# Kernel optimization log

Measured on AMD Instinct MI355X. Metric: run time of the kernel, lower is better.

Reference implementation:

```python
import jax, jax.numpy as jnp
import numpy as np

B, H, S, D = 2, 8, 2048, 64
WINDOW = 3            # local_attention_window (default in torch forward)
FRAC = 0.3            # percentage_frac hardcoded in create_window_tensor call
MASK_FILL = -1.0e9


def window_kernel(window, frac):
    # create_window_tensor: [ (1-f)^n ... (1-f)^1, 1, (1-f)^1 ... (1-f)^n ]
    n = (window - 1) // 2
    side = np.array([(1.0 - frac) ** i for i in range(n, 0, -1)], dtype=np.float32)
    vals = np.concatenate([side, np.array([1.0], np.float32), side[::-1]])
    return jnp.asarray(vals)


def setup_inputs() -> dict:
    key = jax.random.key(0)
    kq, kk, kv = jax.random.split(key, 3)
    queries = jax.random.normal(kq, (B, H, S, D), jnp.float32)
    keys = jax.random.normal(kk, (B, H, S, D), jnp.float32)
    values = jax.random.normal(kv, (B, H, S, D), jnp.float32)
    # causal mask: True positions are filled with -1e9 (masked_fill semantics)
    mask = jnp.triu(jnp.ones((S, S), dtype=bool), 1)[None, None]  # [1,1,S,S]
    # linear_bias: nn.Parameter(torch.zeros(Sk)) created inside forward
    beta = jnp.zeros((S,), jnp.float32)
    return {"queries": queries, "keys": keys, "values": values,
            "beta": beta, "mask": mask}


def reference(queries, keys, values, beta, mask):
    d = keys.shape[-1]
    # scores = Q K^T / sqrt(d)
    scores = jnp.einsum("bhqd,bhkd->bhqk", queries, keys) / jnp.sqrt(
        jnp.asarray(d, queries.dtype))
    scores = jnp.where(mask, jnp.asarray(MASK_FILL, scores.dtype), scores)
    # include_local_attention=True, local_attention_dim_vertical=False:
    # the torch code transposes, conv2d with a [1,W] kernel along the last
    # axis, transposes back -> 1D cross-correlation along the QUERY axis.
    # Kernel is symmetric so correlation == convolution. Zero padding.
    kern = window_kernel(WINDOW, FRAC)
    p = (WINDOW - 1) // 2
    xp = jnp.pad(scores, ((0, 0), (0, 0), (p, p), (0, 0)))
    Sq = scores.shape[2]
    scores = sum(kern[i] * jax.lax.dynamic_slice_in_dim(xp, i, Sq, axis=2)
                 for i in range(WINDOW))
    # linear_bias=True: add zero-initialized per-key-position bias
    scores = scores + beta  # broadcasts over last dim [Sk]
    weights = jax.nn.softmax(scores, axis=-1)
    return jnp.einsum("bhqk,bhkd->bhqd", weights, values)
```

## Files before the change

kernel.cpp:

```cpp
#include <hip/hip_runtime.h>


typedef short bf16x8 __attribute__((ext_vector_type(8)));
typedef float f32x4  __attribute__((ext_vector_type(4)));

constexpr int S_ = 2048;
constexpr int D_ = 64;
constexpr float LOG2E = 1.44269504088896341f;
constexpr float KSC = 0.125f * LOG2E;

__device__ __forceinline__ unsigned pk2(float lo, float hi) {
    union { float f; unsigned u; } a, b;
    a.f = lo; b.f = hi;
    return __builtin_amdgcn_perm(b.u + 0x8000u, a.u + 0x8000u, 0x07060302u);
}

__global__ __launch_bounds__(256)
void cvt8(const float* __restrict__ K, const float* __restrict__ V,
          unsigned short* __restrict__ F)
{
    __shared__ float T[64][68];

    const int bid = blockIdx.x;
    const int hd = bid & 15, tt = bid >> 4;
    const float* Kt = K + ((size_t)hd * S_ + tt * 64) * D_;
    const float* Vt = V + ((size_t)hd * S_ + tt * 64) * D_;
    unsigned short* Ft = F + (size_t)(hd * 32 + tt) * 8192;

    const int t = threadIdx.x;
    const int key = t >> 2, d0 = (t & 3) << 4;

    {
        const float* vp = Vt + key * D_ + d0;
        #pragma unroll
        for (int i = 0; i < 4; ++i) {
            float4 v4 = *(const float4*)(vp + 4 * i);
            T[d0 + 4 * i + 0][key] = v4.x;
            T[d0 + 4 * i + 1][key] = v4.y;
            T[d0 + 4 * i + 2][key] = v4.z;
            T[d0 + 4 * i + 3][key] = v4.w;
        }
    }

    {
        const float* kp = Kt + key * D_ + d0;
        float4 a = *(const float4*)(kp);
        float4 b = *(const float4*)(kp + 4);
        float4 c = *(const float4*)(kp + 8);
        float4 d = *(const float4*)(kp + 12);
        uint4 w0 = make_uint4(pk2(a.x, a.y), pk2(a.z, a.w), pk2(b.x, b.y), pk2(b.z, b.w));
        uint4 w1 = make_uint4(pk2(c.x, c.y), pk2(c.z, c.w), pk2(d.x, d.y), pk2(d.z, d.w));
        const int r5 = key & 31;
        const int kh = key >> 5, mb = (r5 >> 2) & 1;
        const int n = ((r5 >> 3) << 2) | (r5 & 3);
        const int hh = d0 >> 5, qd0 = (d0 >> 3) & 3;
        const int f0 = (kh << 2) | (mb << 1) | hh;
        *(uint4*)(Ft + f0 * 512 + ((qd0 << 4) | n) * 8)       = w0;
        *(uint4*)(Ft + f0 * 512 + (((qd0 + 1) << 4) | n) * 8) = w1;
    }
    __syncthreads();

    #pragma unroll
    for (int s = 0; s < 2; ++s) {
        const int slot = t + s * 256;
        const int fr = slot >> 6, lane = slot & 63;
        const int kh = fr >> 2, mb = fr & 3, n = lane & 15, qd = lane >> 4;
        const float* row = &T[mb * 16 + n][kh * 32 + qd * 8];
        uint4 w = make_uint4(pk2(row[0], row[1]), pk2(row[2], row[3]),
                             pk2(row[4], row[5]), pk2(row[6], row[7]));
        *(uint4*)(Ft + (8 + fr) * 512 + lane * 8) = w;
    }
}

__global__ __launch_bounds__(512, 2)
void attn9(const float* __restrict__ Q, const float* __restrict__ beta,
           const unsigned short* __restrict__ F, float* __restrict__ out)
{
    __shared__ float slab[2][64][72];

    const int bid = blockIdx.x;
    const int hd = bid & 15;
    const int pr = bid >> 4;

    const float* Qh = Q + (size_t)hd * S_ * D_;
    const unsigned short* Fh = F + (size_t)hd * 32 * 8192;

    const int t = threadIdx.x, lane = t & 63;
    const int wv = t >> 6;
    const int kh = wv & 1, par = (wv >> 1) & 1, qh = wv >> 2;
    const int n_l = lane & 15, qd = lane >> 4;

    const int lo = lane * 8;
    int kfo[2][2], vfo[4];
    #pragma unroll
    for (int mb = 0; mb < 2; ++mb)
        #pragma unroll
        for (int hh = 0; hh < 2; ++hh)
            kfo[mb][hh] = ((kh << 2) | (mb << 1) | hh) * 512 + lo;
    #pragma unroll
    for (int mb = 0; mb < 4; ++mb)
        vfo[mb] = (8 + (kh << 2) + mb) * 512 + lo;

    const int kvo = (kh << 5) + (qd << 3);
    const float* bp = beta + kvo;

    for (int p = 0; p < 2; ++p) {
        const int j = p ? (31 - pr) : pr;
        const int q0 = j << 6;
        const int nt = j + 1;
        const int qbase = q0 + (qh << 5);

        auto ld = [&](int tile, bf16x8 (&ka)[2][2], bf16x8 (&vb)[4], float (&bt)[8]) {
            const unsigned short* fp = Fh + (size_t)tile * 8192;
            ka[0][0] = *(const bf16x8*)(fp + kfo[0][0]);
            ka[0][1] = *(const bf16x8*)(fp + kfo[0][1]);
            ka[1][0] = *(const bf16x8*)(fp + kfo[1][0]);
            ka[1][1] = *(const bf16x8*)(fp + kfo[1][1]);
            #pragma unroll
            for (int mb = 0; mb < 4; ++mb)
                vb[mb] = *(const bf16x8*)(fp + vfo[mb]);
            const float* bq = bp + (tile << 6);
            float4 b0 = *(const float4*)(bq);
            float4 b1 = *(const float4*)(bq + 4);
            bt[0] = b0.x * LOG2E; bt[1] = b0.y * LOG2E;
            bt[2] = b0.z * LOG2E; bt[3] = b0.w * LOG2E;
            bt[4] = b1.x * LOG2E; bt[5] = b1.y * LOG2E;
            bt[6] = b1.z * LOG2E; bt[7] = b1.w * LOG2E;
        };

        bf16x8 qb[2][2];
        #pragma unroll
        for (int ng = 0; ng < 2; ++ng) {
            const int q = qbase + (ng << 4) + n_l;
            const float wp = (q > 0) ? 0.7f : 0.0f;
            const float wn = (q + 1 < S_) ? 0.7f : 0.0f;
            const float* qc = Qh + (size_t)q * D_;
            const float* qpp = qc - ((q > 0) ? D_ : 0);
            const float* qnn = qc + ((q + 1 < S_) ? D_ : 0);
            #pragma unroll
            for (int hh = 0; hh < 2; ++hh) {
                const int d0 = (hh << 5) + (qd << 3);
                float4 c0 = *(const float4*)(qc + d0),  c1 = *(const float4*)(qc + d0 + 4);
                float4 p0 = *(const float4*)(qpp + d0), p1 = *(const float4*)(qpp + d0 + 4);
                float4 n0 = *(const float4*)(qnn + d0), n1 = *(const float4*)(qnn + d0 + 4);
                float e0 = fmaf(wn, n0.x, fmaf(wp, p0.x, c0.x));
                float e1 = fmaf(wn, n0.y, fmaf(wp, p0.y, c0.y));
                float e2 = fmaf(wn, n0.z, fmaf(wp, p0.z, c0.z));
                float e3 = fmaf(wn, n0.w, fmaf(wp, p0.w, c0.w));
                float e4 = fmaf(wn, n1.x, fmaf(wp, p1.x, c1.x));
                float e5 = fmaf(wn, n1.y, fmaf(wp, p1.y, c1.y));
                float e6 = fmaf(wn, n1.z, fmaf(wp, p1.z, c1.z));
                float e7 = fmaf(wn, n1.w, fmaf(wp, p1.w, c1.w));
                union { unsigned u[4]; bf16x8 v; } qu;
                qu.u[0] = pk2(e0, e1); qu.u[1] = pk2(e2, e3);
                qu.u[2] = pk2(e4, e5); qu.u[3] = pk2(e6, e7);
                qb[ng][hh] = qu.v;
            }
        }

        f32x4 o[4][2];
        float l[2] = {0.0f, 0.0f};
        #pragma unroll
        for (int mb = 0; mb < 4; ++mb)
            #pragma unroll
            for (int ng = 0; ng < 2; ++ng) o[mb][ng] = (f32x4){0, 0, 0, 0};

        auto comp = [&](int tile, bf16x8 (&ka)[2][2], bf16x8 (&vb)[4], float (&bt)[8]) {
            const f32x4 zz = {0, 0, 0, 0};
            f32x4 acc[2][2];
            #pragma unroll
            for (int mb = 0; mb < 2; ++mb)
                #pragma unroll
                for (int ng = 0; ng < 2; ++ng) {
                    f32x4 a = __builtin_amdgcn_mfma_f32_16x16x32_bf16(ka[mb][0], qb[ng][0], zz, 0, 0, 0);
                    acc[mb][ng] = __builtin_amdgcn_mfma_f32_16x16x32_bf16(ka[mb][1], qb[ng][1], a, 0, 0, 0);
                }
            const bool dm = (tile == nt - 1);
            const int kk = (tile << 6) + kvo;
            union { unsigned u[4]; bf16x8 v; } pf[2];
            #pragma unroll
            for (int ng = 0; ng < 2; ++ng) {
                const int qr = qbase + (ng << 4) + n_l;
                float pv[8];
                float la = 0.0f;
                #pragma unroll
                for (int jj = 0; jj < 8; ++jj) {
                    const int mb = jj >> 2, r = jj & 3;
                    float sv = fmaf(acc[mb][ng][r], KSC, bt[jj]);
                    if (dm) {
                        const int key = kk + jj;
                        if (!((key < qr) || (qr == 0 && key == 0))) sv = -1.0e30f;
                    }
                    pv[jj] = __builtin_amdgcn_exp2f(sv);
                    la += pv[jj];
                }
                l[ng] += la;
                pf[ng].u[0] = pk2(pv[0], pv[1]);
                pf[ng].u[1] = pk2(pv[2], pv[3]);
                pf[ng].u[2] = pk2(pv[4], pv[5]);
                pf[ng].u[3] = pk2(pv[6], pv[7]);
            }
            #pragma unroll
            for (int mb = 0; mb < 4; ++mb)
                #pragma unroll
                for (int ng = 0; ng < 2; ++ng)
                    o[mb][ng] = __builtin_amdgcn_mfma_f32_16x16x32_bf16(vb[mb], pf[ng].v, o[mb][ng], 0, 0, 0);
        };

        bf16x8 kaA[2][2], vbA[4]; float btA[8];
        bf16x8 kaB[2][2], vbB[4]; float btB[8];
        int it = par;
        if (it < nt) {
            ld(it, kaA, vbA, btA);
            if (it + 2 < nt) ld(it + 2, kaB, vbB, btB);
            while (it + 4 < nt) {
                comp(it, kaA, vbA, btA);
                ld(it + 4, kaA, vbA, btA);
                comp(it + 2, kaB, vbB, btB);
                if (it + 6 < nt) ld(it + 6, kaB, vbB, btB);
                it += 4;
            }
            comp(it, kaA, vbA, btA);
            if (it + 2 < nt) comp(it + 2, kaB, vbB, btB);
        }

        #pragma unroll
        for (int ng = 0; ng < 2; ++ng) {
            l[ng] += __shfl_xor(l[ng], 16);
            l[ng] += __shfl_xor(l[ng], 32);
        }
        __syncthreads();
        if (par == 1) {
            #pragma unroll
            for (int ng = 0; ng < 2; ++ng) {
                const int row = (qh << 5) + (ng << 4) + n_l;
                #pragma unroll
                for (int mb = 0; mb < 4; ++mb)
                    *(float4*)&slab[kh][row][(mb << 4) + (qd << 2)] =
                        make_float4(o[mb][ng][0], o[mb][ng][1], o[mb][ng][2], o[mb][ng][3]);
                if (qd == 0) slab[kh][row][64] = l[ng];
            }
        }
        __syncthreads();
        if (par == 0) {
            #pragma unroll
            for (int ng = 0; ng < 2; ++ng) {
                const int row = (qh << 5) + (ng << 4) + n_l;
                #pragma unroll
                for (int mb = 0; mb < 4; ++mb) {
                    float4 pv4 = *(float4*)&slab[kh][row][(mb << 4) + (qd << 2)];
                    o[mb][ng][0] += pv4.x; o[mb][ng][1] += pv4.y;
                    o[mb][ng][2] += pv4.z; o[mb][ng][3] += pv4.w;
                }
                l[ng] += slab[kh][row][64];
                if (kh == 0) {
                    #pragma unroll
                    for (int mb = 0; mb < 4; ++mb)
                        *(float4*)&slab[0][row][(mb << 4) + (qd << 2)] =
                            make_float4(o[mb][ng][0], o[mb][ng][1], o[mb][ng][2], o[mb][ng][3]);
                    if (qd == 0) slab[0][row][64] = l[ng];
                }
            }
        }
        __syncthreads();
        if (par == 0 && kh == 1) {
            #pragma unroll
            for (int ng = 0; ng < 2; ++ng) {
                const int row = (qh << 5) + (ng << 4) + n_l;
                const float inv = 1.0f / (l[ng] + slab[0][row][64]);
                float* op = out + ((size_t)hd * S_ + q0 + row) * D_ + (qd << 2);
                #pragma unroll
                for (int mb = 0; mb < 4; ++mb) {
                    float4 pv4 = *(float4*)&slab[0][row][(mb << 4) + (qd << 2)];
                    *(float4*)(op + (mb << 4)) =
                        make_float4((o[mb][ng][0] + pv4.x) * inv, (o[mb][ng][1] + pv4.y) * inv,
                                    (o[mb][ng][2] + pv4.z) * inv, (o[mb][ng][3] + pv4.w) * inv);
                }
            }
        }
    }
}

extern "C" void kernel_launch(void* const* d_in, const int* in_sizes, int n_in,
                              void* d_out, int out_size, void* d_ws, size_t ws_size,
                              hipStream_t stream) {
    const float* Q    = (const float*)d_in[0];
    const float* K    = (const float*)d_in[1];
    const float* V    = (const float*)d_in[2];
    const float* beta = (const float*)d_in[3];
    float* out = (float*)d_out;

    unsigned short* F = (unsigned short*)d_ws;

    cvt8<<<dim3(512), 256, 0, stream>>>(K, V, F);
    attn9<<<dim3(256), 512, 0, stream>>>(Q, beta, F, out);
}
```

Before: 116.4 us.

## Split key tiles four ways per wave and stage beta in shared memory

The attention kernel changes how work is split across its 8 waves. Before, waves were divided between two query halves and two key-tile parities. Now every wave covers all 64 queries of the block and the key tiles are split four ways, so each K/V fragment load feeds twice as many MFMAs. The beta bias is pre-scaled once into shared memory rather than loaded from global memory per tile. The causal-mask branch becomes a compile-time template specialisation. The cost is a larger accumulator register footprint, more shared memory (a 3-way partial-sum slab plus the beta array), and a longer reduction across waves at the end.

Result: slower. 148.2 us (+27.3%).

```diff
diff --git a/kernel.cpp b/kernel.cpp
--- a/kernel.cpp
+++ b/kernel.cpp
@@ -8,6 +8,8 @@
 constexpr int D_ = 64;
 constexpr float LOG2E = 1.44269504088896341f;
 constexpr float KSC = 0.125f * LOG2E;
+
+template <bool B> struct BC { static constexpr bool v = B; };
 
 __device__ __forceinline__ unsigned pk2(float lo, float hi) {
     union { float f; unsigned u; } a, b;
@@ -73,10 +75,11 @@
 }
 
 __global__ __launch_bounds__(512, 2)
-void attn9(const float* __restrict__ Q, const float* __restrict__ beta,
-           const unsigned short* __restrict__ F, float* __restrict__ out)
+void attn10(const float* __restrict__ Q, const float* __restrict__ beta,
+            const unsigned short* __restrict__ F, float* __restrict__ out)
 {
-    __shared__ float slab[2][64][72];
+    __shared__ float slab[2][3][64][68];
+    __shared__ float bl[S_];
 
     const int bid = blockIdx.x;
     const int hd = bid & 15;
@@ -87,8 +90,12 @@
 
     const int t = threadIdx.x, lane = t & 63;
     const int wv = t >> 6;
-    const int kh = wv & 1, par = (wv >> 1) & 1, qh = wv >> 2;
+    const int kh = wv & 1, par = wv >> 1;
     const int n_l = lane & 15, qd = lane >> 4;
+
+    #pragma unroll
+    for (int i = 0; i < 4; ++i) bl[t + i * 512] = beta[t + i * 512] * LOG2E;
+    __syncthreads();
 
     const int lo = lane * 8;
     int kfo[2][2], vfo[4];
@@ -102,15 +109,13 @@
         vfo[mb] = (8 + (kh << 2) + mb) * 512 + lo;
 
     const int kvo = (kh << 5) + (qd << 3);
-    const float* bp = beta + kvo;
 
     for (int p = 0; p < 2; ++p) {
         const int j = p ? (31 - pr) : pr;
         const int q0 = j << 6;
         const int nt = j + 1;
-        const int qbase = q0 + (qh << 5);
-
-        auto ld = [&](int tile, bf16x8 (&ka)[2][2], bf16x8 (&vb)[4], float (&bt)[8]) {
+
+        auto ld = [&](int tile, bf16x8 (&ka)[2][2], bf16x8 (&vb)[4]) {
             const unsigned short* fp = Fh + (size_t)tile * 8192;
             ka[0][0] = *(const bf16x8*)(fp + kfo[0][0]);
             ka[0][1] = *(const bf16x8*)(fp + kfo[0][1]);
@@ -119,19 +124,12 @@
             #pragma unroll
             for (int mb = 0; mb < 4; ++mb)
                 vb[mb] = *(const bf16x8*)(fp + vfo[mb]);
-            const float* bq = bp + (tile << 6);
-            float4 b0 = *(const float4*)(bq);
-            float4 b1 = *(const float4*)(bq + 4);
-            bt[0] = b0.x * LOG2E; bt[1] = b0.y * LOG2E;
-            bt[2] = b0.z * LOG2E; bt[3] = b0.w * LOG2E;
-            bt[4] = b1.x * LOG2E; bt[5] = b1.y * LOG2E;
-            bt[6] = b1.z * LOG2E; bt[7] = b1.w * LOG2E;
         };
 
-        bf16x8 qb[2][2];
-        #pragma unroll
-        for (int ng = 0; ng < 2; ++ng) {
-            const int q = qbase + (ng << 4) + n_l;
+        bf16x8 qb[4][2];
+        #pragma unroll
+        for (int ng = 0; ng < 4; ++ng) {
+            const int q = q0 + (ng << 4) + n_l;
             const float wp = (q > 0) ? 0.7f : 0.0f;
             const float wn = (q + 1 < S_) ? 0.7f : 0.0f;
             const float* qc = Qh + (size_t)q * D_;
@@ -158,120 +156,129 @@
             }
         }
 
-        f32x4 o[4][2];
-        float l[2] = {0.0f, 0.0f};
+        f32x4 o[4][4];
+        float l[4] = {0.0f, 0.0f, 0.0f, 0.0f};
         #pragma unroll
         for (int mb = 0; mb < 4; ++mb)
             #pragma unroll
-            for (int ng = 0; ng < 2; ++ng) o[mb][ng] = (f32x4){0, 0, 0, 0};
-
-        auto comp = [&](int tile, bf16x8 (&ka)[2][2], bf16x8 (&vb)[4], float (&bt)[8]) {
+            for (int ng = 0; ng < 4; ++ng) o[mb][ng] = (f32x4){0, 0, 0, 0};
+
+        auto comp = [&](int tile, bf16x8 (&ka)[2][2], bf16x8 (&vb)[4], auto dmc) {
+            constexpr bool DM = decltype(dmc)::v;
+            const int kb = (tile << 6) + kvo;
+            float4 b0 = *(const float4*)&bl[kb];
+            float4 b1 = *(const float4*)&bl[kb + 4];
+            const float bt[8] = {b0.x, b0.y, b0.z, b0.w, b1.x, b1.y, b1.z, b1.w};
             const f32x4 zz = {0, 0, 0, 0};
-            f32x4 acc[2][2];
+            f32x4 acc[2][4];
             #pragma unroll
             for (int mb = 0; mb < 2; ++mb)
                 #pragma unroll
-                for (int ng = 0; ng < 2; ++ng) {
+                for (int ng = 0; ng < 4; ++ng) {
                     f32x4 a = __builtin_amdgcn_mfma_f32_16x16x32_bf16(ka[mb][0], qb[ng][0], zz, 0, 0, 0);
                     acc[mb][ng] = __builtin_amdgcn_mfma_f32_16x16x32_bf16(ka[mb][1], qb[ng][1], a, 0, 0, 0);
                 }
-            const bool dm = (tile == nt - 1);
-            const int kk = (tile << 6) + kvo;
-            union { unsigned u[4]; bf16x8 v; } pf[2];
-            #pragma unroll
-            for (int ng = 0; ng < 2; ++ng) {
-                const int qr = qbase + (ng << 4) + n_l;
+            #pragma unroll
+            for (int ng = 0; ng < 4; ++ng) {
                 float pv[8];
                 float la = 0.0f;
                 #pragma unroll
                 for (int jj = 0; jj < 8; ++jj) {
                     const int mb = jj >> 2, r = jj & 3;
                     float sv = fmaf(acc[mb][ng][r], KSC, bt[jj]);
-                    if (dm) {
-                        const int key = kk + jj;
+                    if constexpr (DM) {
+                        const int qr = q0 + (ng << 4) + n_l;
+                        const int key = kb + jj;
                         if (!((key < qr) || (qr == 0 && key == 0))) sv = -1.0e30f;
                     }
                     pv[jj] = __builtin_amdgcn_exp2f(sv);
                     la += pv[jj];
                 }
                 l[ng] += la;
-                pf[ng].u[0] = pk2(pv[0], pv[1]);
-                pf[ng].u[1] = pk2(pv[2], pv[3]);
-                pf[ng].u[2] = pk2(pv[4], pv[5]);
-                pf[ng].u[3] = pk2(pv[6], pv[7]);
-            }
-            #pragma unroll
-            for (int mb = 0; mb < 4; ++mb)
-                #pragma unroll
-                for (int ng = 0; ng < 2; ++ng)
-                    o[mb][ng] = __builtin_amdgcn_mfma_f32_16x16x32_bf16(vb[mb], pf[ng].v, o[mb][ng], 0, 0, 0);
+                union { unsigned u[4]; bf16x8 v; } pf;
+                pf.u[0] = pk2(pv[0], pv[1]);
+                pf.u[1] = pk2(pv[2], pv[3]);
+                pf.u[2] = pk2(pv[4], pv[5]);
+                pf.u[3] = pk2(pv[6], pv[7]);
+                #pragma unroll
+                for (int mb = 0; mb < 4; ++mb)
+                    o[mb][ng] = __builtin_amdgcn_mfma_f32_16x16x32_bf16(vb[mb], pf.v, o[mb][ng], 0, 0, 0);
+            }
         };
 
-        bf16x8 kaA[2][2], vbA[4]; float btA[8];
-        bf16x8 kaB[2][2], vbB[4]; float btB[8];
+        bf16x8 kaA[2][2], vbA[4];
+        bf16x8 kaB[2][2], vbB[4];
         int it = par;
         if (it < nt) {
-            ld(it, kaA, vbA, btA);
-            if (it + 2 < nt) ld(it + 2, kaB, vbB, btB);
-            while (it + 4 < nt) {
-                comp(it, kaA, vbA, btA);
-                ld(it + 4, kaA, vbA, btA);
-                comp(it + 2, kaB, vbB, btB);
-                if (it + 6 < nt) ld(it + 6, kaB, vbB, btB);
-                it += 4;
-            }
-            comp(it, kaA, vbA, btA);
-            if (it + 2 < nt) comp(it + 2, kaB, vbB, btB);
-        }
-
-        #pragma unroll
-        for (int ng = 0; ng < 2; ++ng) {
+            ld(it, kaA, vbA);
+            if (it + 4 < nt) ld(it + 4, kaB, vbB);
+            while (it + 8 < nt) {
+                comp(it, kaA, vbA, BC<false>{});
+                ld(it + 8, kaA, vbA);
+                comp(it + 4, kaB, vbB, BC<false>{});
+                if (it + 12 < nt) ld(it + 12, kaB, vbB);
+                it += 8;
+            }
+            if (it == nt - 1) comp(it, kaA, vbA, BC<true>{});
+            else              comp(it, kaA, vbA, BC<false>{});
+            if (it + 4 < nt) {
+                if (it + 4 == nt - 1) comp(it + 4, kaB, vbB, BC<true>{});
+                else                  comp(it + 4, kaB, vbB, BC<false>{});
+            }
+        }
+
+        #pragma unroll
+        for (int ng = 0; ng < 4; ++ng) {
             l[ng] += __shfl_xor(l[ng], 16);
             l[ng] += __shfl_xor(l[ng], 32);
         }
         __syncthreads();
-        if (par == 1) {
-            #pragma unroll
-            for (int ng = 0; ng < 2; ++ng) {
-                const int row = (qh << 5) + (ng << 4) + n_l;
+        if (par != 0) {
+            const int si = par - 1;
+            #pragma unroll
+            for (int ng = 0; ng < 4; ++ng) {
+                const int row = (ng << 4) + n_l;
                 #pragma unroll
                 for (int mb = 0; mb < 4; ++mb)
-                    *(float4*)&slab[kh][row][(mb << 4) + (qd << 2)] =
+                    *(float4*)&slab[kh][si][row][(mb << 4) + (qd << 2)] =
                         make_float4(o[mb][ng][0], o[mb][ng][1], o[mb][ng][2], o[mb][ng][3]);
-                if (qd == 0) slab[kh][row][64] = l[ng];
+                if (qd == 0) slab[kh][si][row][64] = l[ng];
             }
         }
         __syncthreads();
         if (par == 0) {
             #pragma unroll
-            for (int ng = 0; ng < 2; ++ng) {
-                const int row = (qh << 5) + (ng << 4) + n_l;
+            for (int ng = 0; ng < 4; ++ng) {
+                const int row = (ng << 4) + n_l;
                 #pragma unroll
                 for (int mb = 0; mb < 4; ++mb) {
-                    float4 pv4 = *(float4*)&slab[kh][row][(mb << 4) + (qd << 2)];
-                    o[mb][ng][0] += pv4.x; o[mb][ng][1] += pv4.y;
-                    o[mb][ng][2] += pv4.z; o[mb][ng][3] += pv4.w;
-                }
-                l[ng] += slab[kh][row][64];
-                if (kh == 0) {
+                    #pragma unroll
+                    for (int si = 0; si < 3; ++si) {
+                        float4 pv4 = *(float4*)&slab[kh][si][row][(mb << 4) + (qd << 2)];
+                        o[mb][ng][0] += pv4.x; o[mb][ng][1] += pv4.y;
+                        o[mb][ng][2] += pv4.z; o[mb][ng][3] += pv4.w;
+                    }
+                }
+                l[ng] += slab[kh][0][row][64] + slab[kh][1][row][64] + slab[kh][2][row][64];
+                if (kh == 1) {
                     #pragma unroll
                     for (int mb = 0; mb < 4; ++mb)
-                        *(float4*)&slab[0][row][(mb << 4) + (qd << 2)] =
+                        *(float4*)&slab[1][0][row][(mb << 4) + (qd << 2)] =
                             make_float4(o[mb][ng][0], o[mb][ng][1], o[mb][ng][2], o[mb][ng][3]);
-                    if (qd == 0) slab[0][row][64] = l[ng];
+                    if (qd == 0) slab[1][0][row][64] = l[ng];
                 }
             }
         }
         __syncthreads();
-        if (par == 0 && kh == 1) {
-            #pragma unroll
-            for (int ng = 0; ng < 2; ++ng) {
-                const int row = (qh << 5) + (ng << 4) + n_l;
-                const float inv = 1.0f / (l[ng] + slab[0][row][64]);
+        if (par == 0 && kh == 0) {
+            #pragma unroll
+            for (int ng = 0; ng < 4; ++ng) {
+                const int row = (ng << 4) + n_l;
+                const float inv = 1.0f / (l[ng] + slab[1][0][row][64]);
                 float* op = out + ((size_t)hd * S_ + q0 + row) * D_ + (qd << 2);
                 #pragma unroll
                 for (int mb = 0; mb < 4; ++mb) {
-                    float4 pv4 = *(float4*)&slab[0][row][(mb << 4) + (qd << 2)];
+                    float4 pv4 = *(float4*)&slab[1][0][row][(mb << 4) + (qd << 2)];
                     *(float4*)(op + (mb << 4)) =
                         make_float4((o[mb][ng][0] + pv4.x) * inv, (o[mb][ng][1] + pv4.y) * inv,
                                     (o[mb][ng][2] + pv4.z) * inv, (o[mb][ng][3] + pv4.w) * inv);
@@ -293,5 +300,5 @@
     unsigned short* F = (unsigned short*)d_ws;
 
     cvt8<<<dim3(512), 256, 0, stream>>>(K, V, F);
-    attn9<<<dim3(256), 512, 0, stream>>>(Q, beta, F, out);
+    attn10<<<dim3(256), 512, 0, stream>>>(Q, beta, F, out);
 }
```

## Split paired query tiles into separate blocks, stage beta in LDS, prefetch only K

Applied to the files above, without the earlier changes.

Each block used to process two query tiles (j and 31-j) back to back. Now every block handles one tile, the grid doubles to 512 blocks, and blocks are ordered so the longest tiles start first. The beta bias is pre-scaled into shared memory once per block. The software pipeline now prefetches only the K fragments for the next tile, while V is loaded inside the compute step. Launch bounds are raised to 4 blocks per CU to increase occupancy, at the cost of register pressure and less latency hiding for the V loads.

Result: slower. 133.1 us (+14.3%).

```diff
diff --git a/kernel.cpp b/kernel.cpp
--- a/kernel.cpp
+++ b/kernel.cpp
@@ -8,6 +8,8 @@
 constexpr int D_ = 64;
 constexpr float LOG2E = 1.44269504088896341f;
 constexpr float KSC = 0.125f * LOG2E;
+
+template <bool B> struct BC { static constexpr bool v = B; };
 
 __device__ __forceinline__ unsigned pk2(float lo, float hi) {
     union { float f; unsigned u; } a, b;
@@ -72,15 +74,20 @@
     }
 }
 
-__global__ __launch_bounds__(512, 2)
-void attn9(const float* __restrict__ Q, const float* __restrict__ beta,
-           const unsigned short* __restrict__ F, float* __restrict__ out)
+__global__ __launch_bounds__(512, 4)
+void attn14(const float* __restrict__ Q, const float* __restrict__ beta,
+            const unsigned short* __restrict__ F, float* __restrict__ out)
 {
     __shared__ float slab[2][64][72];
+    __shared__ float bl[S_];
 
     const int bid = blockIdx.x;
     const int hd = bid & 15;
-    const int pr = bid >> 4;
+    const int rest = bid >> 4;
+    const int j = (rest < 16) ? (31 - 2 * rest) : (2 * (rest - 16));
+
+    const int q0 = j << 6;
+    const int nt = j + 1;
 
     const float* Qh = Q + (size_t)hd * S_ * D_;
     const unsigned short* Fh = F + (size_t)hd * 32 * 8192;
@@ -89,6 +96,11 @@
     const int wv = t >> 6;
     const int kh = wv & 1, par = (wv >> 1) & 1, qh = wv >> 2;
     const int n_l = lane & 15, qd = lane >> 4;
+    const int qbase = q0 + (qh << 5);
+
+    #pragma unroll
+    for (int i = 0; i < 4; ++i) bl[t + i * 512] = beta[t + i * 512] * LOG2E;
+    __syncthreads();
 
     const int lo = lane * 8;
     int kfo[2][2], vfo[4];
@@ -102,180 +114,169 @@
         vfo[mb] = (8 + (kh << 2) + mb) * 512 + lo;
 
     const int kvo = (kh << 5) + (qd << 3);
-    const float* bp = beta + kvo;
-
-    for (int p = 0; p < 2; ++p) {
-        const int j = p ? (31 - pr) : pr;
-        const int q0 = j << 6;
-        const int nt = j + 1;
-        const int qbase = q0 + (qh << 5);
-
-        auto ld = [&](int tile, bf16x8 (&ka)[2][2], bf16x8 (&vb)[4], float (&bt)[8]) {
-            const unsigned short* fp = Fh + (size_t)tile * 8192;
-            ka[0][0] = *(const bf16x8*)(fp + kfo[0][0]);
-            ka[0][1] = *(const bf16x8*)(fp + kfo[0][1]);
-            ka[1][0] = *(const bf16x8*)(fp + kfo[1][0]);
-            ka[1][1] = *(const bf16x8*)(fp + kfo[1][1]);
+
+    auto ld_ka = [&](int tile, bf16x8 (&ka)[2][2]) {
+        const unsigned short* fp = Fh + (size_t)tile * 8192;
+        ka[0][0] = *(const bf16x8*)(fp + kfo[0][0]);
+        ka[0][1] = *(const bf16x8*)(fp + kfo[0][1]);
+        ka[1][0] = *(const bf16x8*)(fp + kfo[1][0]);
+        ka[1][1] = *(const bf16x8*)(fp + kfo[1][1]);
+    };
+
+    bf16x8 qb[2][2];
+    #pragma unroll
+    for (int ng = 0; ng < 2; ++ng) {
+        const int q = qbase + (ng << 4) + n_l;
+        const float wp = (q > 0) ? 0.7f : 0.0f;
+        const float wn = (q + 1 < S_) ? 0.7f : 0.0f;
+        const float* qc = Qh + (size_t)q * D_;
+        const float* qpp = qc - ((q > 0) ? D_ : 0);
+        const float* qnn = qc + ((q + 1 < S_) ? D_ : 0);
+        #pragma unroll
+        for (int hh = 0; hh < 2; ++hh) {
+            const int d0 = (hh << 5) + (qd << 3);
+            float4 c0 = *(const float4*)(qc + d0),  c1 = *(const float4*)(qc + d0 + 4);
+            float4 p0 = *(const float4*)(qpp + d0), p1 = *(const float4*)(qpp + d0 + 4);
+            float4 n0 = *(const float4*)(qnn + d0), n1 = *(const float4*)(qnn + d0 + 4);
+            float e0 = fmaf(wn, n0.x, fmaf(wp, p0.x, c0.x));
+            float e1 = fmaf(wn, n0.y, fmaf(wp, p0.y, c0.y));
+            float e2 = fmaf(wn, n0.z, fmaf(wp, p0.z, c0.z));
+            float e3 = fmaf(wn, n0.w, fmaf(wp, p0.w, c0.w));
+            float e4 = fmaf(wn, n1.x, fmaf(wp, p1.x, c1.x));
+            float e5 = fmaf(wn, n1.y, fmaf(wp, p1.y, c1.y));
+            float e6 = fmaf(wn, n1.z, fmaf(wp, p1.z, c1.z));
+            float e7 = fmaf(wn, n1.w, fmaf(wp, p1.w, c1.w));
+            union { unsigned u[4]; bf16x8 v; } qu;
+            qu.u[0] = pk2(e0, e1); qu.u[1] = pk2(e2, e3);
+            qu.u[2] = pk2(e4, e5); qu.u[3] = pk2(e6, e7);
+            qb[ng][hh] = qu.v;
+        }
+    }
+
+    f32x4 o[4][2];
+    float l[2] = {0.0f, 0.0f};
+    #pragma unroll
+    for (int mb = 0; mb < 4; ++mb)
+        #pragma unroll
+        for (int ng = 0; ng < 2; ++ng) o[mb][ng] = (f32x4){0, 0, 0, 0};
+
+    auto comp = [&](int tile, bf16x8 (&kaC)[2][2], bf16x8 (&kaN)[2][2], auto prc) {
+        constexpr bool PRE = decltype(prc)::v;
+        const int kb = (tile << 6) + kvo;
+        const unsigned short* fp = Fh + (size_t)tile * 8192;
+        bf16x8 vb[4];
+        #pragma unroll
+        for (int mb = 0; mb < 4; ++mb)
+            vb[mb] = *(const bf16x8*)(fp + vfo[mb]);
+        float4 b0 = *(const float4*)&bl[kb];
+        float4 b1 = *(const float4*)&bl[kb + 4];
+        const float bt[8] = {b0.x, b0.y, b0.z, b0.w, b1.x, b1.y, b1.z, b1.w};
+        const f32x4 zz = {0, 0, 0, 0};
+        f32x4 acc[2][2];
+        #pragma unroll
+        for (int mb = 0; mb < 2; ++mb)
+            #pragma unroll
+            for (int ng = 0; ng < 2; ++ng) {
+                f32x4 a = __builtin_amdgcn_mfma_f32_16x16x32_bf16(kaC[mb][0], qb[ng][0], zz, 0, 0, 0);
+                acc[mb][ng] = __builtin_amdgcn_mfma_f32_16x16x32_bf16(kaC[mb][1], qb[ng][1], a, 0, 0, 0);
+            }
+        if constexpr (PRE) ld_ka(tile + 2, kaN);
+        const bool dm = (tile == nt - 1);
+        #pragma unroll
+        for (int ng = 0; ng < 2; ++ng) {
+            const int qr = qbase + (ng << 4) + n_l;
+            float pv[8];
+            float la = 0.0f;
+            #pragma unroll
+            for (int jj = 0; jj < 8; ++jj) {
+                const int mb = jj >> 2, r = jj & 3;
+                float sv = fmaf(acc[mb][ng][r], KSC, bt[jj]);
+                if (dm) {
+                    const int key = kb + jj;
+                    if (!((key < qr) || (qr == 0 && key == 0))) sv = -1.0e30f;
+                }
+                pv[jj] = __builtin_amdgcn_exp2f(sv);
+                la += pv[jj];
+            }
+            l[ng] += la;
+            union { unsigned u[4]; bf16x8 v; } pf;
+            pf.u[0] = pk2(pv[0], pv[1]);
+            pf.u[1] = pk2(pv[2], pv[3]);
+            pf.u[2] = pk2(pv[4], pv[5]);
+            pf.u[3] = pk2(pv[6], pv[7]);
             #pragma unroll
             for (int mb = 0; mb < 4; ++mb)
-                vb[mb] = *(const bf16x8*)(fp + vfo[mb]);
-            const float* bq = bp + (tile << 6);
-            float4 b0 = *(const float4*)(bq);
-            float4 b1 = *(const float4*)(bq + 4);
-            bt[0] = b0.x * LOG2E; bt[1] = b0.y * LOG2E;
-            bt[2] = b0.z * LOG2E; bt[3] = b0.w * LOG2E;
-            bt[4] = b1.x * LOG2E; bt[5] = b1.y * LOG2E;
-            bt[6] = b1.z * LOG2E; bt[7] = b1.w * LOG2E;
-        };
-
-        bf16x8 qb[2][2];
-        #pragma unroll
-        for (int ng = 0; ng < 2; ++ng) {
-            const int q = qbase + (ng << 4) + n_l;
-            const float wp = (q > 0) ? 0.7f : 0.0f;
-            const float wn = (q + 1 < S_) ? 0.7f : 0.0f;
-            const float* qc = Qh + (size_t)q * D_;
-            const float* qpp = qc - ((q > 0) ? D_ : 0);
-            const float* qnn = qc + ((q + 1 < S_) ? D_ : 0);
-            #pragma unroll
-            for (int hh = 0; hh < 2; ++hh) {
-                const int d0 = (hh << 5) + (qd << 3);
-                float4 c0 = *(const float4*)(qc + d0),  c1 = *(const float4*)(qc + d0 + 4);
-                float4 p0 = *(const float4*)(qpp + d0), p1 = *(const float4*)(qpp + d0 + 4);
-                float4 n0 = *(const float4*)(qnn + d0), n1 = *(const float4*)(qnn + d0 + 4);
-                float e0 = fmaf(wn, n0.x, fmaf(wp, p0.x, c0.x));
-                float e1 = fmaf(wn, n0.y, fmaf(wp, p0.y, c0.y));
-                float e2 = fmaf(wn, n0.z, fmaf(wp, p0.z, c0.z));
-                float e3 = fmaf(wn, n0.w, fmaf(wp, p0.w, c0.w));
-                float e4 = fmaf(wn, n1.x, fmaf(wp, p1.x, c1.x));
-                float e5 = fmaf(wn, n1.y, fmaf(wp, p1.y, c1.y));
-                float e6 = fmaf(wn, n1.z, fmaf(wp, p1.z, c1.z));
-                float e7 = fmaf(wn, n1.w, fmaf(wp, p1.w, c1.w));
-                union { unsigned u[4]; bf16x8 v; } qu;
-                qu.u[0] = pk2(e0, e1); qu.u[1] = pk2(e2, e3);
-                qu.u[2] = pk2(e4, e5); qu.u[3] = pk2(e6, e7);
-                qb[ng][hh] = qu.v;
-            }
-        }
-
-        f32x4 o[4][2];
-        float l[2] = {0.0f, 0.0f};
-        #pragma unroll
-        for (int mb = 0; mb < 4; ++mb)
-            #pragma unroll
-            for (int ng = 0; ng < 2; ++ng) o[mb][ng] = (f32x4){0, 0, 0, 0};
-
-        auto comp = [&](int tile, bf16x8 (&ka)[2][2], bf16x8 (&vb)[4], float (&bt)[8]) {
-            const f32x4 zz = {0, 0, 0, 0};
-            f32x4 acc[2][2];
-            #pragma unroll
-            for (int mb = 0; mb < 2; ++mb)
-                #pragma unroll
-                for (int ng = 0; ng < 2; ++ng) {
-                    f32x4 a = __builtin_amdgcn_mfma_f32_16x16x32_bf16(ka[mb][0], qb[ng][0], zz, 0, 0, 0);
-                    acc[mb][ng] = __builtin_amdgcn_mfma_f32_16x16x32_bf16(ka[mb][1], qb[ng][1], a, 0, 0, 0);
-                }
-            const bool dm = (tile == nt - 1);
-            const int kk = (tile << 6) + kvo;
-            union { unsigned u[4]; bf16x8 v; } pf[2];
-            #pragma unroll
-            for (int ng = 0; ng < 2; ++ng) {
-                const int qr = qbase + (ng << 4) + n_l;
-                float pv[8];
-                float la = 0.0f;
-                #pragma unroll
-                for (int jj = 0; jj < 8; ++jj) {
-                    const int mb = jj >> 2, r = jj & 3;
-                    float sv = fmaf(acc[mb][ng][r], KSC, bt[jj]);
-                    if (dm) {
-                        const int key = kk + jj;
-                        if (!((key < qr) || (qr == 0 && key == 0))) sv = -1.0e30f;
-                    }
-                    pv[jj] = __builtin_amdgcn_exp2f(sv);
-                    la += pv[jj];
-                }
-                l[ng] += la;
-                pf[ng].u[0] = pk2(pv[0], pv[1]);
-                pf[ng].u[1] = pk2(pv[2], pv[3]);
-                pf[ng].u[2] = pk2(pv[4], pv[5]);
-                pf[ng].u[3] = pk2(pv[6], pv[7]);
-            }
+                o[mb][ng] = __builtin_amdgcn_mfma_f32_16x16x32_bf16(vb[mb], pf.v, o[mb][ng], 0, 0, 0);
+        }
+    };
+
+    bf16x8 kaA[2][2], kaB[2][2];
+    int it = par;
+    if (it < nt) {
+        ld_ka(it, kaA);
+        while (it + 4 < nt) {
+            comp(it,     kaA, kaB, BC<true>{});
+            comp(it + 2, kaB, kaA, BC<true>{});
+            it += 4;
+        }
+        if (it + 2 < nt) {
+            comp(it,     kaA, kaB, BC<true>{});
+            comp(it + 2, kaB, kaA, BC<false>{});
+        } else {
+            comp(it, kaA, kaB, BC<false>{});
+        }
+    }
+
+    #pragma unroll
+    for (int ng = 0; ng < 2; ++ng) {
+        l[ng] += __shfl_xor(l[ng], 16);
+        l[ng] += __shfl_xor(l[ng], 32);
+    }
+    if (par == 1) {
+        #pragma unroll
+        for (int ng = 0; ng < 2; ++ng) {
+            const int row = (qh << 5) + (ng << 4) + n_l;
             #pragma unroll
             for (int mb = 0; mb < 4; ++mb)
-                #pragma unroll
-                for (int ng = 0; ng < 2; ++ng)
-                    o[mb][ng] = __builtin_amdgcn_mfma_f32_16x16x32_bf16(vb[mb], pf[ng].v, o[mb][ng], 0, 0, 0);
-        };
-
-        bf16x8 kaA[2][2], vbA[4]; float btA[8];
-        bf16x8 kaB[2][2], vbB[4]; float btB[8];
-        int it = par;
-        if (it < nt) {
-            ld(it, kaA, vbA, btA);
-            if (it + 2 < nt) ld(it + 2, kaB, vbB, btB);
-            while (it + 4 < nt) {
-                comp(it, kaA, vbA, btA);
-                ld(it + 4, kaA, vbA, btA);
-                comp(it + 2, kaB, vbB, btB);
-                if (it + 6 < nt) ld(it + 6, kaB, vbB, btB);
-                it += 4;
-            }
-            comp(it, kaA, vbA, btA);
-            if (it + 2 < nt) comp(it + 2, kaB, vbB, btB);
-        }
-
-        #pragma unroll
-        for (int ng = 0; ng < 2; ++ng) {
-            l[ng] += __shfl_xor(l[ng], 16);
-            l[ng] += __shfl_xor(l[ng], 32);
-        }
-        __syncthreads();
-        if (par == 1) {
-            #pragma unroll
-            for (int ng = 0; ng < 2; ++ng) {
-                const int row = (qh << 5) + (ng << 4) + n_l;
+                *(float4*)&slab[kh][row][(mb << 4) + (qd << 2)] =
+                    make_float4(o[mb][ng][0], o[mb][ng][1], o[mb][ng][2], o[mb][ng][3]);
+            if (qd == 0) slab[kh][row][64] = l[ng];
+        }
+    }
+    __syncthreads();
+    if (par == 0) {
+        #pragma unroll
+        for (int ng = 0; ng < 2; ++ng) {
+            const int row = (qh << 5) + (ng << 4) + n_l;
+            #pragma unroll
+            for (int mb = 0; mb < 4; ++mb) {
+                float4 pv4 = *(float4*)&slab[kh][row][(mb << 4) + (qd << 2)];
+                o[mb][ng][0] += pv4.x; o[mb][ng][1] += pv4.y;
+                o[mb][ng][2] += pv4.z; o[mb][ng][3] += pv4.w;
+            }
+            l[ng] += slab[kh][row][64];
+            if (kh == 0) {
                 #pragma unroll
                 for (int mb = 0; mb < 4; ++mb)
-                    *(float4*)&slab[kh][row][(mb << 4) + (qd << 2)] =
+                    *(float4*)&slab[0][row][(mb << 4) + (qd << 2)] =
                         make_float4(o[mb][ng][0], o[mb][ng][1], o[mb][ng][2], o[mb][ng][3]);
-                if (qd == 0) slab[kh][row][64] = l[ng];
-            }
-        }
-        __syncthreads();
-        if (par == 0) {
-            #pragma unroll
-            for (int ng = 0; ng < 2; ++ng) {
-                const int row = (qh << 5) + (ng << 4) + n_l;
-                #pragma unroll
-                for (int mb = 0; mb < 4; ++mb) {
-                    float4 pv4 = *(float4*)&slab[kh][row][(mb << 4) + (qd << 2)];
-                    o[mb][ng][0] += pv4.x; o[mb][ng][1] += pv4.y;
-                    o[mb][ng][2] += pv4.z; o[mb][ng][3] += pv4.w;
-                }
-                l[ng] += slab[kh][row][64];
-                if (kh == 0) {
-                    #pragma unroll
-                    for (int mb = 0; mb < 4; ++mb)
-                        *(float4*)&slab[0][row][(mb << 4) + (qd << 2)] =
-                            make_float4(o[mb][ng][0], o[mb][ng][1], o[mb][ng][2], o[mb][ng][3]);
-                    if (qd == 0) slab[0][row][64] = l[ng];
-                }
-            }
-        }
-        __syncthreads();
-        if (par == 0 && kh == 1) {
-            #pragma unroll
-            for (int ng = 0; ng < 2; ++ng) {
-                const int row = (qh << 5) + (ng << 4) + n_l;
-                const float inv = 1.0f / (l[ng] + slab[0][row][64]);
-                float* op = out + ((size_t)hd * S_ + q0 + row) * D_ + (qd << 2);
-                #pragma unroll
-                for (int mb = 0; mb < 4; ++mb) {
-                    float4 pv4 = *(float4*)&slab[0][row][(mb << 4) + (qd << 2)];
-                    *(float4*)(op + (mb << 4)) =
-                        make_float4((o[mb][ng][0] + pv4.x) * inv, (o[mb][ng][1] + pv4.y) * inv,
-                                    (o[mb][ng][2] + pv4.z) * inv, (o[mb][ng][3] + pv4.w) * inv);
-                }
+                if (qd == 0) slab[0][row][64] = l[ng];
+            }
+        }
+    }
+    __syncthreads();
+    if (par == 0 && kh == 1) {
+        #pragma unroll
+        for (int ng = 0; ng < 2; ++ng) {
+            const int row = (qh << 5) + (ng << 4) + n_l;
+            const float inv = 1.0f / (l[ng] + slab[0][row][64]);
+            float* op = out + ((size_t)hd * S_ + q0 + row) * D_ + (qd << 2);
+            #pragma unroll
+            for (int mb = 0; mb < 4; ++mb) {
+                float4 pv4 = *(float4*)&slab[0][row][(mb << 4) + (qd << 2)];
+                *(float4*)(op + (mb << 4)) =
+                    make_float4((o[mb][ng][0] + pv4.x) * inv, (o[mb][ng][1] + pv4.y) * inv,
+                                (o[mb][ng][2] + pv4.z) * inv, (o[mb][ng][3] + pv4.w) * inv);
             }
         }
     }
@@ -293,5 +294,5 @@
     unsigned short* F = (unsigned short*)d_ws;
 
     cvt8<<<dim3(512), 256, 0, stream>>>(K, V, F);
-    attn9<<<dim3(256), 512, 0, stream>>>(Q, beta, F, out);
-}
+    attn14<<<dim3(512), 512, 0, stream>>>(Q, beta, F, out);
+}
```
